# Optimization experiments

Hardware: AMD Instinct MI355X
Metric: run time of the kernel (lower is better)

## Reference

```python
import jax, jax.numpy as jnp
import numpy as np

NUM_ROUTERS = 8
K = 2
IN_DIM = 384
HID = 64
TEMP = 1.0
AUX_COEF = 0.05
EPS = 1e-12


def _l2norm(v, axis=-1):
    n = jnp.sqrt(jnp.sum(v * v, axis=axis, keepdims=True))
    return v / jnp.maximum(n, EPS)


def setup_inputs() -> dict:
    key = jax.random.key(0)
    ks = jax.random.split(key, 10)
    B, E = 8192, 1024
    s = 1.0 / np.sqrt(IN_DIM)
    return {
        "x": jax.random.normal(ks[0], (B, IN_DIM), jnp.float32),
        "reasoning_embeddings": jax.random.normal(ks[1], (E, IN_DIM), jnp.float32),
        "random_num": jax.random.uniform(ks[2], (B, 1), jnp.float32),
        "gate_w": jax.random.normal(ks[3], (IN_DIM, NUM_ROUTERS), jnp.float32) * s,
        "gate_b": jnp.zeros((NUM_ROUTERS,), jnp.float32),
        "Uw": jax.random.normal(ks[4], (NUM_ROUTERS, IN_DIM, HID), jnp.float32) * s,
        "Ub": jnp.zeros((NUM_ROUTERS, HID), jnp.float32),
        "Vw": jax.random.normal(ks[5], (NUM_ROUTERS, IN_DIM, HID), jnp.float32) * s,
        "Vb": jnp.zeros((NUM_ROUTERS, HID), jnp.float32),
    }


def reference(x, reasoning_embeddings, random_num, gate_w, gate_b, Uw, Ub, Vw, Vb):
    B = x.shape[0]
    # gate
    logits = x @ gate_w + gate_b                              # [B, R]
    probs = jax.nn.softmax(logits, axis=-1)
    topk_vals, topk_idxs = jax.lax.top_k(logits, K)           # [B, K]
    topk_mask = jax.nn.one_hot(topk_idxs, NUM_ROUTERS).sum(axis=1)  # [B, R]
    aux_loss = NUM_ROUTERS * (probs.mean(0) * topk_mask.mean(0)).sum() * AUX_COEF

    # all routers, batched (replaces the per-(i,j) python loop)
    xu = _l2norm(jnp.einsum("bd,rdh->rbh", x, Uw) + Ub[:, None, :])          # [R, B, H]
    ev = _l2norm(jnp.einsum("ed,rdh->reh", reasoning_embeddings, Vw) + Vb[:, None, :])  # [R, E, H]
    scores = jnp.einsum("rbh,reh->rbe", xu, ev)               # [R, B, E]
    all_out = jax.nn.softmax(scores / TEMP, axis=-1)          # [R, B, E]

    # gather top-k experts per sample
    all_out_b = jnp.transpose(all_out, (1, 0, 2))             # [B, R, E]
    router_outputs = jnp.take_along_axis(all_out_b, topk_idxs[:, :, None], axis=1)  # [B, K, E]

    gate_weights = jax.nn.softmax(topk_vals, axis=-1)[:, :, None]  # [B, K, 1]
    rea_probs = jnp.sum(router_outputs * gate_weights, axis=1)     # [B, E]

    # categorical sampling via inverse-CDF
    scores_cumsum = jnp.cumsum(rea_probs, axis=1)
    selected_index = jnp.argmax((scores_cumsum > random_num).astype(jnp.float32), axis=1)  # [B]
    log_probs = jnp.log(rea_probs[jnp.arange(B), selected_index])[:, None]  # [B, 1]
    return selected_index, log_probs, aux_loss
```

## Files before the change

### kernel.cpp

```cpp
#include <hip/hip_runtime.h>
#include <math.h>

#define B 8192
#define E 1024
#define D 384
#define H 64
#define R 8
#define NCHUNK 16
#define CHUNK_E 64
#define NPOS 17408
#define NROW 25600

#define WS_CNT    0u
#define WS_CUR    32u
#define WS_PS     64u
#define WS_OFFS   96u
#define WS_TOP2   256u
#define WS_GW     65792u
#define WS_POSM   131328u
#define WS_LIST   196864u
#define WS_EVN    266496u
#define WS_XUN    2363648u
#define WS_C      6820096u
#define WS_BUFA   7934208u
#define WS_BUFB   14487808u

__global__ __launch_bounds__(256) void k_gate(
    const float* __restrict__ x, const float* __restrict__ gate_w,
    const float* __restrict__ gate_b, int2* __restrict__ top2,
    float2* __restrict__ gwv, int* __restrict__ counts, float* __restrict__ ps)
{
  __shared__ __align__(16) float gwT[R * 388];
  __shared__ float psl[R];
  __shared__ int   cl[R];
  int tid = threadIdx.x;
  for (int idx = tid; idx < D * R; idx += 256) {
    int k = idx >> 3, r = idx & 7;
    gwT[r * 388 + k] = gate_w[idx];
  }
  if (tid < R) { psl[tid] = 0.f; cl[tid] = 0; }
  __syncthreads();

  int l = tid & 63;
  int r = tid & 7;
  int b = blockIdx.x * 32 + (tid >> 3);
  float acc = gate_b[r];
  const float4* x4 = (const float4*)(x + (size_t)b * D);
  const float*  gr = gwT + r * 388;
#pragma unroll 4
  for (int q = 0; q < 96; ++q) {
    float4 xv = x4[q];
    float4 gv = *(const float4*)&gr[q * 4];
    acc = fmaf(xv.x, gv.x, acc);
    acc = fmaf(xv.y, gv.y, acc);
    acc = fmaf(xv.z, gv.z, acc);
    acc = fmaf(xv.w, gv.w, acc);
  }
  float lv[R];
#pragma unroll
  for (int rr = 0; rr < R; ++rr) lv[rr] = __shfl(acc, (l & ~7) + rr);
  int i0 = 0; float v0 = lv[0];
#pragma unroll
  for (int rr = 1; rr < R; ++rr) if (lv[rr] > v0) { v0 = lv[rr]; i0 = rr; }
  int i1 = (i0 == 0) ? 1 : 0; float v1 = lv[i1];
#pragma unroll
  for (int rr = 0; rr < R; ++rr)
    if (rr != i0 && lv[rr] > v1) { v1 = lv[rr]; i1 = rr; }
  float se = 0.f;
#pragma unroll
  for (int rr = 0; rr < R; ++rr) se += expf(lv[rr] - v0);
  float p = expf(acc - v0) / se;
  if (r == 0) {
    float e10 = expf(v1 - v0);
    top2[b] = make_int2(i0, i1);
    gwv[b]  = make_float2(1.f / (1.f + e10), e10 / (1.f + e10));
  }
  float pa = p;
  int   ca = (r == i0 ? 1 : 0) + (r == i1 ? 1 : 0);
#pragma unroll
  for (int m = 8; m < 64; m <<= 1) {
    pa += __shfl_xor(pa, m);
    ca += __shfl_xor(ca, m);
  }
  if (l < 8) { atomicAdd(&psl[r], pa); atomicAdd(&cl[r], ca); }
  __syncthreads();
  if (tid < R) { atomicAdd(&ps[tid], psl[tid]); atomicAdd(&counts[tid], cl[tid]); }
}

__global__ __launch_bounds__(256) void k_scatter(
    const int2* __restrict__ top2, const int* __restrict__ counts,
    const float* __restrict__ ps, int* __restrict__ cursors,
    int* __restrict__ list, int2* __restrict__ posmap,
    int* __restrict__ offs_g, float* __restrict__ out_aux)
{
  __shared__ int lc[R];
  __shared__ int lbase[R];
  __shared__ int offs[R];
  int tid = threadIdx.x;
  if (tid < R) lc[tid] = 0;
  __syncthreads();
  if (tid == 0) {
    int o = 0;
    for (int r2 = 0; r2 < R; ++r2) { offs[r2] = o; o += (min(counts[r2], B) + 127) & ~127; }
  }
  __syncthreads();
  int b = min(blockIdx.x * 256 + tid, B - 1);
  int2 t = top2[b];
  t.x &= 7; t.y &= 7;
  int p0 = atomicAdd(&lc[t.x], 1);
  int p1 = atomicAdd(&lc[t.y], 1);
  __syncthreads();
  if (tid < R) lbase[tid] = atomicAdd(&cursors[tid], lc[tid]);
  __syncthreads();
  int i0 = min(offs[t.x] + lbase[t.x] + p0, NPOS - 1);
  int i1 = min(offs[t.y] + lbase[t.y] + p1, NPOS - 1);
  list[i0] = b * 2 + 0;
  list[i1] = b * 2 + 1;
  posmap[b] = make_int2(i0, i1);
  if (blockIdx.x == 0 && tid == 0) {
    float s = 0.f;
    for (int r2 = 0; r2 < R; ++r2) {
      s += (ps[r2] / (float)B) * ((float)min(counts[r2], B) / (float)B);
      offs_g[r2] = offs[r2];
    }
    out_aux[0] = (float)R * s * 0.05f;
  }
}

__global__ __launch_bounds__(256) void k_projgemm(
    const float* __restrict__ re, const float* __restrict__ x,
    const float* __restrict__ Vw, const float* __restrict__ Uw,
    const int* __restrict__ list, const int* __restrict__ counts,
    const int* __restrict__ offs, float* __restrict__ bufA,
    float* __restrict__ bufB)
{
  __shared__ __align__(16) float At[64 * 64];
  __shared__ __align__(16) float Wt[64 * 64];
  int tid = threadIdx.x;
  int bid = blockIdx.x;
  int tile = bid >> 1, ks = bid & 1;
  int rowg0 = tile * 64;

  int srow = tid & 63, kq = tid >> 6;
  const float* Wsrc;
  const float* arow;
  if (tile < 128) {
    Wsrc = Vw + (size_t)(rowg0 >> 10) * (D * H);
    arow = re + (size_t)((rowg0 & 1023) + srow) * D;
  } else {
    int pos0 = rowg0 - 8192;
    int tot = offs[R - 1] + ((min(counts[R - 1], B) + 127) & ~127);
    if (pos0 >= tot) return;
    int r = 0;
    for (int rr = 0; rr < R; ++rr) if (pos0 >= offs[rr]) r = rr;
    Wsrc = Uw + (size_t)r * (D * H);
    int gl = list[min(pos0 + srow, NPOS - 1)];
    gl = min(max(gl, 0), 2 * B - 1);
    arow = x + (size_t)(gl >> 1) * D;
  }

  int tr = tid >> 4, tc = tid & 15;
  float acc[4][4];
#pragma unroll
  for (int i = 0; i < 4; ++i)
#pragma unroll
    for (int j = 0; j < 4; ++j) acc[i][j] = 0.f;

  for (int kt = 0; kt < 3; ++kt) {
    int kb = ks * 192 + kt * 64;
    __syncthreads();
#pragma unroll
    for (int q = 0; q < 4; ++q) {
      float4 v = *(const float4*)&arow[kb + (kq + 4 * q) * 4];
      int k0 = (kq + 4 * q) * 4;
      At[(k0 + 0) * 64 + srow] = v.x;
      At[(k0 + 1) * 64 + srow] = v.y;
      At[(k0 + 2) * 64 + srow] = v.z;
      At[(k0 + 3) * 64 + srow] = v.w;
    }
#pragma unroll
    for (int q = 0; q < 4; ++q) {
      int idx = tid + 256 * q;
      int k = idx >> 4, h4 = idx & 15;
      *(float4*)&Wt[k * 64 + h4 * 4] = *(const float4*)&Wsrc[(size_t)(kb + k) * H + h4 * 4];
    }
    __syncthreads();
#pragma unroll 8
    for (int k = 0; k < 64; ++k) {
      float4 a4 = *(const float4*)&At[k * 64 + tr * 4];
      float4 w4 = *(const float4*)&Wt[k * 64 + tc * 4];
      const float* ap = (const float*)&a4;
      const float* wp = (const float*)&w4;
#pragma unroll
      for (int i = 0; i < 4; ++i)
#pragma unroll
        for (int j = 0; j < 4; ++j) acc[i][j] = fmaf(ap[i], wp[j], acc[i][j]);
    }
  }
  float* dst = (ks ? bufB : bufA) + (size_t)rowg0 * H;
#pragma unroll
  for (int i = 0; i < 4; ++i) {
    float4 o;
    o.x = acc[i][0]; o.y = acc[i][1]; o.z = acc[i][2]; o.w = acc[i][3];
    *(float4*)&dst[(tr * 4 + i) * H + tc * 4] = o;
  }
}

__global__ __launch_bounds__(256) void k_projfin(
    const float* __restrict__ bufA, const float* __restrict__ bufB,
    const float* __restrict__ Vb, const float* __restrict__ Ub,
    const int* __restrict__ offs, float* __restrict__ evnT,
    float* __restrict__ xunP)
{
  int tid = threadIdx.x;
  int lane = tid & 63;
  int row0 = blockIdx.x * 32 + (tid >> 6) * 8;
  bool isE = row0 < 8192;
  int r = 0;
  if (isE) {
    r = row0 >> 10;
  } else {
    int pos = row0 - 8192;
    for (int rr = 0; rr < R; ++rr) if (pos >= offs[rr]) r = rr;
  }
  float bias = isE ? Vb[r * H + lane] : Ub[r * H + lane];
#pragma unroll
  for (int i = 0; i < 8; ++i) {
    int row = row0 + i;
    float s = bufA[(size_t)row * H + lane] + bufB[(size_t)row * H + lane] + bias;
    float ss = s * s;
#pragma unroll
    for (int m = 1; m < 64; m <<= 1) ss += __shfl_xor(ss, m);
    float v = s / fmaxf(sqrtf(ss), 1e-12f);
    if (isE) evnT[(size_t)(r * 64 + lane) * 1024 + (row & 1023)] = v;
    else     xunP[(size_t)(row - 8192) * H + lane] = v;
  }
}

__global__ __launch_bounds__(256) void k_pass1(
    const float* __restrict__ evnT, const float* __restrict__ xunP,
    const int* __restrict__ counts, const int* __restrict__ offs,
    float* __restrict__ C)
{
  __shared__ __align__(16) float Xt[32 * 128];
  __shared__ __align__(16) float Et[32 * 128];
  int tid = threadIdx.x;
  int bid = blockIdx.x;
  int et    = bid & 7;
  int stile = (bid >> 3) & 63;
  int r     = bid >> 9;
  int cnt = min(counts[r], B);
  if (cnt <= 0 || stile * 128 >= cnt) return;
  int off = offs[r] + stile * 128;
  int n = min(128, cnt - stile * 128);
  int ebase = et * 128;

  int sg = tid >> 4, egr = tid & 15;
  float acc[8][8];
#pragma unroll
  for (int i = 0; i < 8; ++i)
#pragma unroll
    for (int j = 0; j < 8; ++j) acc[i][j] = 0.f;

  int srow = tid >> 1, shalf = tid & 1;
  int src = min(srow, n - 1);
  const float4* xsrc = (const float4*)(xunP + (size_t)(off + src) * H);

  for (int kst = 0; kst < 2; ++kst) {
    __syncthreads();
    {
#pragma unroll
      for (int q = 0; q < 4; ++q) {
        float4 v = xsrc[kst * 8 + shalf * 4 + q];
        int hb = shalf * 16 + q * 4;
        Xt[(hb + 0) * 128 + srow] = v.x;
        Xt[(hb + 1) * 128 + srow] = v.y;
        Xt[(hb + 2) * 128 + srow] = v.z;
        Xt[(hb + 3) * 128 + srow] = v.w;
      }
    }
    {
#pragma unroll
      for (int q = 0; q < 4; ++q) {
        int idx = tid + 256 * q;
        int h = idx >> 5, e4 = idx & 31;
        *(float4*)&Et[h * 128 + e4 * 4] =
            *(const float4*)(evnT + (size_t)(r * 64 + kst * 32 + h) * 1024 + ebase + e4 * 4);
      }
    }
    __syncthreads();
#pragma unroll 4
    for (int k = 0; k < 32; ++k) {
      float4 xa = *(const float4*)&Xt[k * 128 + sg * 4];
      float4 xb = *(const float4*)&Xt[k * 128 + 64 + sg * 4];
      float4 ea = *(const float4*)&Et[k * 128 + egr * 4];
      float4 eb = *(const float4*)&Et[k * 128 + 64 + egr * 4];
      const float* pa = (const float*)&xa;
      const float* pb = (const float*)&xb;
      const float* qa = (const float*)&ea;
      const float* qb = (const float*)&eb;
#pragma unroll
      for (int i = 0; i < 4; ++i)
#pragma unroll
        for (int j = 0; j < 4; ++j) {
          acc[i][j]         = fmaf(pa[i], qa[j], acc[i][j]);
          acc[i][j + 4]     = fmaf(pa[i], qb[j], acc[i][j + 4]);
          acc[i + 4][j]     = fmaf(pb[i], qa[j], acc[i + 4][j]);
          acc[i + 4][j + 4] = fmaf(pb[i], qb[j], acc[i + 4][j + 4]);
        }
    }
  }

#pragma unroll
  for (int i = 0; i < 8; ++i) {
    float cA = __expf(acc[i][0]) + __expf(acc[i][1]) + __expf(acc[i][2]) + __expf(acc[i][3]);
    float cB = __expf(acc[i][4]) + __expf(acc[i][5]) + __expf(acc[i][6]) + __expf(acc[i][7]);
#pragma unroll
    for (int m = 1; m < 16; m <<= 1) {
      cA += __shfl_xor(cA, m);
      cB += __shfl_xor(cB, m);
    }
    int s = (i < 4) ? (sg * 4 + i) : (64 + sg * 4 + i - 4);
    if (egr == 0 && s < n) {
      C[(size_t)(off + s) * NCHUNK + et * 2]     = cA;
      C[(size_t)(off + s) * NCHUNK + et * 2 + 1] = cB;
    }
  }
}

__global__ __launch_bounds__(256) void k_pass2(
    const float* __restrict__ evnT, const float* __restrict__ xunP,
    const float* __restrict__ C, const int2* __restrict__ top2,
    const int2* __restrict__ posmap, const float2* __restrict__ gwv,
    const float* __restrict__ rnd, float* __restrict__ out)
{
  int tid = threadIdx.x;
  int lane = tid & 63;
  int b = blockIdx.x * 4 + (tid >> 6);
  if (b >= B) return;
  int2 t2 = top2[b];
  t2.x &= 7; t2.y &= 7;
  int2 pm = posmap[b];
  pm.x = min(max(pm.x, 0), NPOS - 1);
  pm.y = min(max(pm.y, 0), NPOS - 1);
  float2 gw = gwv[b];
  float rv = rnd[b];

  const float4* C04 = (const float4*)(C + (size_t)pm.x * NCHUNK);
  const float4* C14 = (const float4*)(C + (size_t)pm.y * NCHUNK);
  float c0[NCHUNK], c1[NCHUNK];
#pragma unroll
  for (int q = 0; q < 4; ++q) {
    float4 v0 = C04[q], v1 = C14[q];
    c0[q*4+0]=v0.x; c0[q*4+1]=v0.y; c0[q*4+2]=v0.z; c0[q*4+3]=v0.w;
    c1[q*4+0]=v1.x; c1[q*4+1]=v1.y; c1[q*4+2]=v1.z; c1[q*4+3]=v1.w;
  }
  float S0 = 0.f, S1 = 0.f;
#pragma unroll
  for (int j = 0; j < NCHUNK; ++j) { S0 += c0[j]; S1 += c1[j]; }
  float a0 = gw.x / S0, a1 = gw.y / S1;
  int cstar = -1; float prefix = 0.f; float run = 0.f;
#pragma unroll
  for (int j = 0; j < NCHUNK; ++j) {
    float nrun = run + (c0[j] * a0 + c1[j] * a1);
    if (cstar < 0 && nrun > rv) { cstar = j; prefix = run; }
    run = nrun;
  }
  float rtgt = rv;
  if (cstar < 0) { cstar = 0; prefix = 0.f; rtgt = -1.0f; }

  float xu0 = xunP[(size_t)pm.x * H + lane];
  float xu1 = xunP[(size_t)pm.y * H + lane];
  const float* E0 = evnT + (size_t)t2.x * 64 * 1024 + cstar * CHUNK_E + lane;
  const float* E1 = evnT + (size_t)t2.y * 64 * 1024 + cstar * CHUNK_E + lane;
  float d0 = 0.f, d1 = 0.f;
#pragma unroll 16
  for (int h = 0; h < 64; ++h) {
    float w0 = __shfl(xu0, h);
    float w1 = __shfl(xu1, h);
    d0 = fmaf(E0[(size_t)h * 1024], w0, d0);
    d1 = fmaf(E1[(size_t)h * 1024], w1, d1);
  }
  float rea = __expf(d0) * a0 + __expf(d1) * a1;
  float sc = rea;
#pragma unroll
  for (int d = 1; d < 64; d <<= 1) {
    float o = __shfl_up(sc, d);
    if (lane >= d) sc += o;
  }
  float cum = prefix + sc;
  unsigned long long m2 = __ballot(cum > rtgt);
  int estar = (m2 == 0ull) ? 63 : (int)__builtin_ctzll(m2);
  float p = __shfl(rea, estar);
  if (lane == 0) {
    int sel = cstar * CHUNK_E + estar;
    out[b]     = (float)sel;
    out[B + b] = logf(p);
  }
}

extern "C" void kernel_launch(void* const* d_in, const int* in_sizes, int n_in,
                              void* d_out, int out_size, void* d_ws, size_t ws_size,
                              hipStream_t stream)
{
  (void)in_sizes; (void)n_in; (void)out_size; (void)ws_size;
  const float* x      = (const float*)d_in[0];
  const float* re     = (const float*)d_in[1];
  const float* rnd    = (const float*)d_in[2];
  const float* gate_w = (const float*)d_in[3];
  const float* gate_b = (const float*)d_in[4];
  const float* Uw     = (const float*)d_in[5];
  const float* Ub     = (const float*)d_in[6];
  const float* Vw     = (const float*)d_in[7];
  const float* Vb     = (const float*)d_in[8];
  char* ws = (char*)d_ws;
  int*    counts  = (int*)(ws + WS_CNT);
  int*    cursors = (int*)(ws + WS_CUR);
  float*  ps      = (float*)(ws + WS_PS);
  int*    offs    = (int*)(ws + WS_OFFS);
  int2*   top2    = (int2*)(ws + WS_TOP2);
  float2* gwv     = (float2*)(ws + WS_GW);
  int2*   posmap  = (int2*)(ws + WS_POSM);
  int*    list    = (int*)(ws + WS_LIST);
  float*  evnT    = (float*)(ws + WS_EVN);
  float*  xunP    = (float*)(ws + WS_XUN);
  float*  Cc      = (float*)(ws + WS_C);
  float*  bufA    = (float*)(ws + WS_BUFA);
  float*  bufB    = (float*)(ws + WS_BUFB);
  float* out = (float*)d_out;

  hipMemsetAsync(ws, 0, 128, stream);
  k_gate    <<<256,  256, 0, stream>>>(x, gate_w, gate_b, top2, gwv, counts, ps);
  k_scatter <<<32,   256, 0, stream>>>(top2, counts, ps, cursors, list, posmap, offs, out + 2 * B);
  k_projgemm<<<800,  256, 0, stream>>>(re, x, Vw, Uw, list, counts, offs, bufA, bufB);
  k_projfin <<<800,  256, 0, stream>>>(bufA, bufB, Vb, Ub, offs, evnT, xunP);
  k_pass1   <<<4096, 256, 0, stream>>>(evnT, xunP, counts, offs, Cc);
  k_pass2   <<<2048, 256, 0, stream>>>(evnT, xunP, Cc, top2, posmap, gwv, rnd, out);
}
```

Baseline: 177.0 us.

## Replace global atomics with per-block partials and chunk-tile the expert embedding layout

The gate kernel now writes per-block router counts and probability sums instead of doing global atomics. The scatter kernel computes deterministic prefix offsets from those partials, which removes the memset and the global cursor atomics. The normalized embedding buffer moves from a [R,H,E] transpose to [R,chunk,H,64] tiles, so that pass2's per-chunk column reads and pass1's tile loads touch contiguous 16KB blocks. In exchange, every scatter block redundantly scans all 256 partials.

```diff
diff --git a/kernel.cpp b/kernel.cpp
--- a/kernel.cpp
+++ b/kernel.cpp
@@ -11,24 +11,24 @@
 #define NPOS 17408
 #define NROW 25600
 
-#define WS_CNT    0u
-#define WS_CUR    32u
-#define WS_PS     64u
-#define WS_OFFS   96u
-#define WS_TOP2   256u
-#define WS_GW     65792u
-#define WS_POSM   131328u
-#define WS_LIST   196864u
-#define WS_EVN    266496u
-#define WS_XUN    2363648u
-#define WS_C      6820096u
-#define WS_BUFA   7934208u
-#define WS_BUFB   14487808u
+#define WS_GCNT   0u
+#define WS_GPS    8192u
+#define WS_CNT    16384u
+#define WS_OFFS   16416u
+#define WS_TOP2   16448u
+#define WS_GW     81984u
+#define WS_POSM   147520u
+#define WS_LIST   213056u
+#define WS_EVN    282688u
+#define WS_XUN    2379840u
+#define WS_C      6836288u
+#define WS_BUFA   7950400u
+#define WS_BUFB   14504000u
 
 __global__ __launch_bounds__(256) void k_gate(
     const float* __restrict__ x, const float* __restrict__ gate_w,
     const float* __restrict__ gate_b, int2* __restrict__ top2,
-    float2* __restrict__ gwv, int* __restrict__ counts, float* __restrict__ ps)
+    float2* __restrict__ gwv, int* __restrict__ gcnt, float* __restrict__ gps)
 {
   __shared__ __align__(16) float gwT[R * 388];
   __shared__ float psl[R];
@@ -84,44 +84,75 @@
   }
   if (l < 8) { atomicAdd(&psl[r], pa); atomicAdd(&cl[r], ca); }
   __syncthreads();
-  if (tid < R) { atomicAdd(&ps[tid], psl[tid]); atomicAdd(&counts[tid], cl[tid]); }
+  if (tid < R) {
+    gcnt[blockIdx.x * R + tid] = cl[tid];
+    gps [blockIdx.x * R + tid] = psl[tid];
+  }
 }
 
 __global__ __launch_bounds__(256) void k_scatter(
-    const int2* __restrict__ top2, const int* __restrict__ counts,
-    const float* __restrict__ ps, int* __restrict__ cursors,
-    int* __restrict__ list, int2* __restrict__ posmap,
-    int* __restrict__ offs_g, float* __restrict__ out_aux)
-{
-  __shared__ int lc[R];
-  __shared__ int lbase[R];
-  __shared__ int offs[R];
-  int tid = threadIdx.x;
-  if (tid < R) lc[tid] = 0;
+    const int2* __restrict__ top2, const int* __restrict__ gcnt,
+    const float* __restrict__ gps, int* __restrict__ counts_g,
+    int* __restrict__ offs_g, int* __restrict__ list,
+    int2* __restrict__ posmap, float* __restrict__ out_aux)
+{
+  __shared__ int   pcs[2048];
+  __shared__ float pfs[2048];
+  __shared__ int cnt[R], pre[R], offs[R], lc[R];
+  __shared__ float psum[R];
+  int tid = threadIdx.x;
+  int g = blockIdx.x;
+  {
+    const int4* s4 = (const int4*)gcnt;
+    int4* d4 = (int4*)pcs;
+    d4[tid]       = s4[tid];
+    d4[tid + 256] = s4[tid + 256];
+    const float4* f4 = (const float4*)gps;
+    float4* e4 = (float4*)pfs;
+    e4[tid]       = f4[tid];
+    e4[tid + 256] = f4[tid + 256];
+  }
+  __syncthreads();
+  if (tid < R) {
+    int c = 0, pr = 0;
+    for (int gg = 0; gg < 256; ++gg) {
+      int v = pcs[gg * 8 + tid];
+      if (gg < g) pr += v;
+      c += v;
+    }
+    cnt[tid] = min(c, B);
+    pre[tid] = pr;
+    lc[tid] = 0;
+    if (g == 0) {
+      float s = 0.f;
+      for (int gg = 0; gg < 256; ++gg) s += pfs[gg * 8 + tid];
+      psum[tid] = s;
+    }
+  }
   __syncthreads();
   if (tid == 0) {
     int o = 0;
-    for (int r2 = 0; r2 < R; ++r2) { offs[r2] = o; o += (min(counts[r2], B) + 127) & ~127; }
+    for (int r2 = 0; r2 < R; ++r2) { offs[r2] = o; o += (cnt[r2] + 127) & ~127; }
   }
   __syncthreads();
-  int b = min(blockIdx.x * 256 + tid, B - 1);
-  int2 t = top2[b];
-  t.x &= 7; t.y &= 7;
-  int p0 = atomicAdd(&lc[t.x], 1);
-  int p1 = atomicAdd(&lc[t.y], 1);
-  __syncthreads();
-  if (tid < R) lbase[tid] = atomicAdd(&cursors[tid], lc[tid]);
-  __syncthreads();
-  int i0 = min(offs[t.x] + lbase[t.x] + p0, NPOS - 1);
-  int i1 = min(offs[t.y] + lbase[t.y] + p1, NPOS - 1);
-  list[i0] = b * 2 + 0;
-  list[i1] = b * 2 + 1;
-  posmap[b] = make_int2(i0, i1);
-  if (blockIdx.x == 0 && tid == 0) {
+  if (tid < 32) {
+    int b = g * 32 + tid;
+    int2 t = top2[b];
+    t.x &= 7; t.y &= 7;
+    int p0 = atomicAdd(&lc[t.x], 1);
+    int p1 = atomicAdd(&lc[t.y], 1);
+    int i0 = min(offs[t.x] + pre[t.x] + p0, NPOS - 1);
+    int i1 = min(offs[t.y] + pre[t.y] + p1, NPOS - 1);
+    list[i0] = b * 2 + 0;
+    list[i1] = b * 2 + 1;
+    posmap[b] = make_int2(i0, i1);
+  }
+  if (g == 0 && tid == 0) {
     float s = 0.f;
     for (int r2 = 0; r2 < R; ++r2) {
-      s += (ps[r2] / (float)B) * ((float)min(counts[r2], B) / (float)B);
-      offs_g[r2] = offs[r2];
+      s += (psum[r2] / (float)B) * ((float)cnt[r2] / (float)B);
+      counts_g[r2] = cnt[r2];
+      offs_g[r2]  = offs[r2];
     }
     out_aux[0] = (float)R * s * 0.05f;
   }
@@ -209,7 +240,7 @@
 __global__ __launch_bounds__(256) void k_projfin(
     const float* __restrict__ bufA, const float* __restrict__ bufB,
     const float* __restrict__ Vb, const float* __restrict__ Ub,
-    const int* __restrict__ offs, float* __restrict__ evnT,
+    const int* __restrict__ offs, float* __restrict__ evnC,
     float* __restrict__ xunP)
 {
   int tid = threadIdx.x;
@@ -232,13 +263,17 @@
 #pragma unroll
     for (int m = 1; m < 64; m <<= 1) ss += __shfl_xor(ss, m);
     float v = s / fmaxf(sqrtf(ss), 1e-12f);
-    if (isE) evnT[(size_t)(r * 64 + lane) * 1024 + (row & 1023)] = v;
-    else     xunP[(size_t)(row - 8192) * H + lane] = v;
+    if (isE) {
+      int e = row & 1023;
+      evnC[(((size_t)(r * 16 + (e >> 6)) * 64 + lane) * 64) + (e & 63)] = v;
+    } else {
+      xunP[(size_t)(row - 8192) * H + lane] = v;
+    }
   }
 }
 
 __global__ __launch_bounds__(256) void k_pass1(
-    const float* __restrict__ evnT, const float* __restrict__ xunP,
+    const float* __restrict__ evnC, const float* __restrict__ xunP,
     const int* __restrict__ counts, const int* __restrict__ offs,
     float* __restrict__ C)
 {
@@ -253,7 +288,6 @@
   if (cnt <= 0 || stile * 128 >= cnt) return;
   int off = offs[r] + stile * 128;
   int n = min(128, cnt - stile * 128);
-  int ebase = et * 128;
 
   int sg = tid >> 4, egr = tid & 15;
   float acc[8][8];
@@ -284,8 +318,9 @@
       for (int q = 0; q < 4; ++q) {
         int idx = tid + 256 * q;
         int h = idx >> 5, e4 = idx & 31;
+        int c = (et << 1) + (e4 >> 4);
         *(float4*)&Et[h * 128 + e4 * 4] =
-            *(const float4*)(evnT + (size_t)(r * 64 + kst * 32 + h) * 1024 + ebase + e4 * 4);
+            *(const float4*)&evnC[(((size_t)(r * 16 + c) * 64) + kst * 32 + h) * 64 + (e4 & 15) * 4];
       }
     }
     __syncthreads();
@@ -329,7 +364,7 @@
 }
 
 __global__ __launch_bounds__(256) void k_pass2(
-    const float* __restrict__ evnT, const float* __restrict__ xunP,
+    const float* __restrict__ evnC, const float* __restrict__ xunP,
     const float* __restrict__ C, const int2* __restrict__ top2,
     const int2* __restrict__ posmap, const float2* __restrict__ gwv,
     const float* __restrict__ rnd, float* __restrict__ out)
@@ -371,15 +406,15 @@
 
   float xu0 = xunP[(size_t)pm.x * H + lane];
   float xu1 = xunP[(size_t)pm.y * H + lane];
-  const float* E0 = evnT + (size_t)t2.x * 64 * 1024 + cstar * CHUNK_E + lane;
-  const float* E1 = evnT + (size_t)t2.y * 64 * 1024 + cstar * CHUNK_E + lane;
+  const float* E0 = evnC + ((size_t)(t2.x * 16 + cstar) * 4096) + lane;
+  const float* E1 = evnC + ((size_t)(t2.y * 16 + cstar) * 4096) + lane;
   float d0 = 0.f, d1 = 0.f;
 #pragma unroll 16
   for (int h = 0; h < 64; ++h) {
     float w0 = __shfl(xu0, h);
     float w1 = __shfl(xu1, h);
-    d0 = fmaf(E0[(size_t)h * 1024], w0, d0);
-    d1 = fmaf(E1[(size_t)h * 1024], w1, d1);
+    d0 = fmaf(E0[h * 64], w0, d0);
+    d1 = fmaf(E1[h * 64], w1, d1);
   }
   float rea = __expf(d0) * a0 + __expf(d1) * a1;
   float sc = rea;
@@ -414,26 +449,25 @@
   const float* Vw     = (const float*)d_in[7];
   const float* Vb     = (const float*)d_in[8];
   char* ws = (char*)d_ws;
+  int*    gcnt    = (int*)(ws + WS_GCNT);
+  float*  gps     = (float*)(ws + WS_GPS);
   int*    counts  = (int*)(ws + WS_CNT);
-  int*    cursors = (int*)(ws + WS_CUR);
-  float*  ps      = (float*)(ws + WS_PS);
   int*    offs    = (int*)(ws + WS_OFFS);
   int2*   top2    = (int2*)(ws + WS_TOP2);
   float2* gwv     = (float2*)(ws + WS_GW);
   int2*   posmap  = (int2*)(ws + WS_POSM);
   int*    list    = (int*)(ws + WS_LIST);
-  float*  evnT    = (float*)(ws + WS_EVN);
+  float*  evnC    = (float*)(ws + WS_EVN);
   float*  xunP    = (float*)(ws + WS_XUN);
   float*  Cc      = (float*)(ws + WS_C);
   float*  bufA    = (float*)(ws + WS_BUFA);
   float*  bufB    = (float*)(ws + WS_BUFB);
   float* out = (float*)d_out;
 
-  hipMemsetAsync(ws, 0, 128, stream);
-  k_gate    <<<256,  256, 0, stream>>>(x, gate_w, gate_b, top2, gwv, counts, ps);
-  k_scatter <<<32,   256, 0, stream>>>(top2, counts, ps, cursors, list, posmap, offs, out + 2 * B);
+  k_gate    <<<256,  256, 0, stream>>>(x, gate_w, gate_b, top2, gwv, gcnt, gps);
+  k_scatter <<<256,  256, 0, stream>>>(top2, gcnt, gps, counts, offs, list, posmap, out + 2 * B);
   k_projgemm<<<800,  256, 0, stream>>>(re, x, Vw, Uw, list, counts, offs, bufA, bufB);
-  k_projfin <<<800,  256, 0, stream>>>(bufA, bufB, Vb, Ub, offs, evnT, xunP);
-  k_pass1   <<<4096, 256, 0, stream>>>(evnT, xunP, counts, offs, Cc);
-  k_pass2   <<<2048, 256, 0, stream>>>(evnT, xunP, Cc, top2, posmap, gwv, rnd, out);
-}
+  k_projfin <<<800,  256, 0, stream>>>(bufA, bufB, Vb, Ub, offs, evnC, xunP);
+  k_pass1   <<<4096, 256, 0, stream>>>(evnC, xunP, counts, offs, Cc);
+  k_pass2   <<<2048, 256, 0, stream>>>(evnC, xunP, Cc, top2, posmap, gwv, rnd, out);
+}
```

Result: slower. 181.9 us (+2.8%).
